# Optimization experiments

Hardware: AMD Instinct MI355X
Metric: run time of the kernel (lower is better)

Reference implementation:

```python
import jax, jax.numpy as jnp
import numpy as np

LMAX = 5
DIMS = [2 * l + 1 for l in range(LMAX + 1)]
S = sum(d * d for d in DIMS)  # 286 = sum_l (2l+1)^2 (mul_l = dim_l = 2l+1)
F_IN, F_OUT = 128, 128
B = 512
N_GRID = 512


def setup_inputs() -> dict:
    key = jax.random.key(0)
    k1, k2, k3 = jax.random.split(key, 3)
    # x: signal over SO(3) irreps, shape (B, f_in, S)
    x = jax.random.normal(k1, (B, F_IN, S), dtype=jnp.float32)
    # w: learned spatial filter, shape (f_in, f_out, n_grid) (nn.Parameter, normal init)
    w = jax.random.normal(k2, (F_IN, F_OUT, N_GRID), dtype=jnp.float32)
    # D: flattened Wigner-D buffer, shape (n_grid, S). Stand-in random values;
    # the forward math is identical to the true Wigner-D buffer.
    D = jax.random.normal(k3, (N_GRID, S), dtype=jnp.float32)
    return {"x": x, "w": w, "D": D}


def _so3_linear(x, psi):
    """e3nn o3.Linear over so3_irreps(LMAX) with external weights psi.

    Per degree l: x_l (B, f_in, 2l+1 [mul], 2l+1 [dim]),
    psi_l (f_in, f_out, mul_in, mul_out); mix multiplicities and f channels,
    with fan-in normalization 1/sqrt(f_in * mul_in).
    """
    bsz = x.shape[0]
    outs = []
    off = 0
    for l in range(LMAX + 1):
        d = 2 * l + 1
        blk = d * d
        x_l = x[:, :, off:off + blk].reshape(bsz, F_IN, d, d)
        w_l = psi[:, :, off:off + blk].reshape(F_IN, F_OUT, d, d)
        scale = 1.0 / np.sqrt(F_IN * d).astype(np.float32)
        y_l = jnp.einsum('bxui,xyuv->byvi', x_l, w_l) * scale
        outs.append(y_l.reshape(bsz, F_OUT, blk))
        off += blk
    return jnp.concatenate(outs, axis=-1)


def reference(x, w, D):
    # project spatial filter into harmonic (Fourier) domain
    psi = jnp.einsum('ni,xyn->xyi', D, w) / np.float32(np.sqrt(N_GRID))
    return _so3_linear(x, psi)
```

## Files before the change

### kernel.cpp

```cpp
#include <hip/hip_runtime.h>
#include <hip/hip_bf16.h>


#define NT 256
typedef __bf16 bf16x8 __attribute__((ext_vector_type(8)));
typedef float f32x4 __attribute__((ext_vector_type(4)));
typedef unsigned int u32;

__device__ __forceinline__ void gload_lds16(const void* g, void* l) {
  __builtin_amdgcn_global_load_lds(
      (const __attribute__((address_space(1))) u32*)g,
      (__attribute__((address_space(3))) u32*)l, 16, 0, 0);
}

__device__ __forceinline__ void decode_s(int s, int& off, int& d) {
  if (s >= 165)      { off = 165; d = 11; }
  else if (s >= 84)  { off = 84;  d = 9; }
  else if (s >= 35)  { off = 35;  d = 7; }
  else if (s >= 10)  { off = 10;  d = 5; }
  else if (s >= 1)   { off = 1;   d = 3; }
  else               { off = 0;   d = 1; }
}

template<int D, int OFF>
__device__ __forceinline__ void build_one(const float* __restrict__ X,
                                          __hip_bfloat16* __restrict__ A,
                                          int b, __hip_bfloat16* sm) {
  const float* src = X + (size_t)b * (128 * 286) + OFF;
  for (int e = threadIdx.x; e < 128 * D * D; e += NT) {
    const int x = e / (D * D), r = e - x * (D * D);
    sm[e] = __float2bfloat16(src[x * 286 + r]);
  }
  __syncthreads();
  __hip_bfloat16* dst = A + (size_t)65536 * OFF + (size_t)b * (D * 128 * D);
  for (int o = threadIdx.x; o < D * 128 * D; o += NT) {
    const int i = o / (128 * D);
    const int rem = o - i * (128 * D);
    const int x = rem / D, u = rem - x * D;
    dst[o] = sm[x * D * D + u * D + i];
  }
}

__global__ __launch_bounds__(NT)
void prep_all(const float* __restrict__ w, const float* __restrict__ Dm,
              const float* __restrict__ X,
              __hip_bfloat16* __restrict__ wb, __hip_bfloat16* __restrict__ DT,
              __hip_bfloat16* __restrict__ A) {
  __shared__ __hip_bfloat16 sm[128 * 121];
  const int bx = blockIdx.x;
  if (bx < 4096) {
    const int t = bx * NT + threadIdx.x;
    const float4 a = reinterpret_cast<const float4*>(w)[t * 2];
    const float4 b = reinterpret_cast<const float4*>(w)[t * 2 + 1];
    __hip_bfloat16 v[8];
    v[0] = __float2bfloat16(a.x); v[1] = __float2bfloat16(a.y);
    v[2] = __float2bfloat16(a.z); v[3] = __float2bfloat16(a.w);
    v[4] = __float2bfloat16(b.x); v[5] = __float2bfloat16(b.y);
    v[6] = __float2bfloat16(b.z); v[7] = __float2bfloat16(b.w);
    *reinterpret_cast<bf16x8*>(&wb[t * 8]) = *reinterpret_cast<bf16x8*>(v);
  } else if (bx < 4864) {
    const int e = (bx - 4096) * NT + threadIdx.x;
    const int s = e >> 9, g = e & 511;
    DT[e] = (s < 286) ? __float2bfloat16(Dm[g * 286 + s]) : __float2bfloat16(0.0f);
  } else {
    const int b2 = bx - 4864;
    if (b2 < 512)       build_one<11, 165>(X, A, b2, sm);
    else if (b2 < 1024) build_one<9, 84>(X, A, b2 - 512, sm);
    else if (b2 < 1536) build_one<7, 35>(X, A, b2 - 1024, sm);
    else if (b2 < 2048) build_one<5, 10>(X, A, b2 - 1536, sm);
    else if (b2 < 2560) build_one<3, 1>(X, A, b2 - 2048, sm);
    else                build_one<1, 0>(X, A, b2 - 2560, sm);
  }
}

__device__ __forceinline__ void load_frags(
    const __hip_bfloat16* sA, const __hip_bfloat16* sB,
    int wr, int wc, int r15, int khi, bf16x8 (&af)[4][2], bf16x8 (&bf)[4][2]) {
#pragma unroll
  for (int m = 0; m < 4; ++m)
#pragma unroll
    for (int kk = 0; kk < 2; ++kk) {
      const int row = wr * 64 + m * 16 + r15;
      const int slot = (kk * 4 + khi) ^ (row & 7);
      af[m][kk] = *reinterpret_cast<const bf16x8*>(&sA[row * 64 + slot * 8]);
    }
#pragma unroll
  for (int n = 0; n < 4; ++n)
#pragma unroll
    for (int kk = 0; kk < 2; ++kk) {
      const int row = wc * 64 + n * 16 + r15;
      const int slot = (kk * 4 + khi) ^ (row & 7);
      bf[n][kk] = *reinterpret_cast<const bf16x8*>(&sB[row * 64 + slot * 8]);
    }
}

__device__ __forceinline__ void do_mfma(
    const bf16x8 (&af)[4][2], const bf16x8 (&bf)[4][2], f32x4 (&acc)[4][4]) {
#pragma unroll
  for (int kk = 0; kk < 2; ++kk)
#pragma unroll
    for (int m = 0; m < 4; ++m)
#pragma unroll
      for (int n = 0; n < 4; ++n)
        acc[m][n] = __builtin_amdgcn_mfma_f32_16x16x32_bf16(
            af[m][kk], bf[n][kk], acc[m][n], 0, 0, 0);
}

__device__ __forceinline__ void stage_tile(
    const __hip_bfloat16* __restrict__ Ap, const __hip_bfloat16* __restrict__ Bp,
    int LDK, int ktv, int m0, int n0, int tid, int wave,
    __hip_bfloat16* sA, __hip_bfloat16* sB) {
#pragma unroll
  for (int c = 0; c < 4; ++c) {
    const int q = c * 256 + tid;
    const int row = q >> 3, slot = q & 7;
    const int scol = ((slot ^ (row & 7)) << 3);
    gload_lds16(&Ap[(m0 + row) * LDK + ktv + scol], &sA[(c * 256 + wave * 64) << 3]);
    gload_lds16(&Bp[(n0 + row) * LDK + ktv + scol], &sB[(c * 256 + wave * 64) << 3]);
  }
}

__global__ __launch_bounds__(NT)
void psi_mfma(const __hip_bfloat16* __restrict__ wb,
              const __hip_bfloat16* __restrict__ DT,
              __hip_bfloat16* __restrict__ PT) {
  const int m0 = blockIdx.x * 128, n0 = blockIdx.y * 128;

  __shared__ __hip_bfloat16 sA[2][128 * 64];
  __shared__ __hip_bfloat16 sB[2][128 * 64];

  const int tid = threadIdx.x;
  const int lane = tid & 63, wave = tid >> 6;
  const int wr = wave & 1, wc = wave >> 1;
  const int r15 = lane & 15, khi = lane >> 4;

  f32x4 acc[4][4] = {};
  bf16x8 af[4][2], bf[4][2];

  stage_tile(wb, DT, 512, 0, m0, n0, tid, wave, sA[0], sB[0]);
  __syncthreads();
  int cur = 0;
  for (int t = 0; t < 8; ++t) {
    if (t + 1 < 8)
      stage_tile(wb, DT, 512, (t + 1) << 6, m0, n0, tid, wave, sA[cur ^ 1], sB[cur ^ 1]);
    load_frags(sA[cur], sB[cur], wr, wc, r15, khi, af, bf);
    do_mfma(af, bf, acc);
    if (t + 1 < 8) { __syncthreads(); cur ^= 1; }
  }

#pragma unroll
  for (int n = 0; n < 4; ++n) {
    const int s = n0 + wc * 64 + n * 16 + r15;
    if (s >= 286) continue;
    int off, d;
    decode_s(s, off, d);
    const int rel = s - off;
    const int u = rel / d, v = rel - u * d;
    const float scale = 1.0f / (256.0f * sqrtf((float)d));
    __hip_bfloat16* Pl = PT + off * 16384;
    const int Kd = 128 * d;
#pragma unroll
    for (int m = 0; m < 4; ++m)
#pragma unroll
      for (int j = 0; j < 4; ++j) {
        const int row = m0 + wr * 64 + m * 16 + khi * 4 + j;
        const int x = row >> 7, y = row & 127;
        Pl[(y * d + v) * Kd + (x * d + u)] = __float2bfloat16(acc[m][n][j] * scale);
      }
  }
}

template<int D, int OFF>
__device__ __forceinline__ void tile_body(
    const __hip_bfloat16* __restrict__ Aall,
    const __hip_bfloat16* __restrict__ PTall,
    float* __restrict__ out, int bx,
    __hip_bfloat16* s0A, __hip_bfloat16* s0B,
    __hip_bfloat16* s1A, __hip_bfloat16* s1B) {
  const int tid = threadIdx.x;
  const int lane = tid & 63, wave = tid >> 6;
  const int wr = wave & 1, wc = wave >> 1;
  const int r15 = lane & 15, khi = lane >> 4;

  constexpr int Kn = 128 * D;
  constexpr int nk = 2 * D;
  const int bm = bx % (4 * D);
  const int bn = bx / (4 * D);
  const __hip_bfloat16* A  = Aall  + 65536 * OFF;
  const __hip_bfloat16* BT = PTall + 16384 * OFF;
  const int m0 = bm * 128, n0 = bn * 128;

  const int q0 = tid;
  f32x4 acc[4][4] = {};
  bf16x8 af[4][2], bf[4][2];

  __hip_bfloat16 *curA = s0A, *curB = s0B, *nxtA = s1A, *nxtB = s1B;

#pragma unroll
  for (int c = 0; c < 4; ++c) {
    const int q = c * 256 + q0;
    const int row = q >> 3, slot = q & 7;
    const int scol = ((slot ^ (row & 7)) << 3);
    gload_lds16(&A[(m0 + row) * Kn + scol], &curA[(c * 256 + wave * 64) << 3]);
    gload_lds16(&BT[(n0 + row) * Kn + scol], &curB[(c * 256 + wave * 64) << 3]);
  }

  for (int t = 0; t < nk; ++t) {
    if (t + 1 < nk) {
      const int kt = (t + 1) << 6;
#pragma unroll
      for (int c = 0; c < 4; ++c) {
        const int q = c * 256 + q0;
        const int row = q >> 3, slot = q & 7;
        const int scol = ((slot ^ (row & 7)) << 3);
        gload_lds16(&A[(m0 + row) * Kn + kt + scol], &nxtA[(c * 256 + wave * 64) << 3]);
        gload_lds16(&BT[(n0 + row) * Kn + kt + scol], &nxtB[(c * 256 + wave * 64) << 3]);
      }
      asm volatile("s_waitcnt vmcnt(8)" ::: "memory");
    } else {
      asm volatile("s_waitcnt vmcnt(0)" ::: "memory");
    }
    __builtin_amdgcn_s_barrier();
    asm volatile("" ::: "memory");

    load_frags(curA, curB, wr, wc, r15, khi, af, bf);
    __builtin_amdgcn_s_setprio(1);
    do_mfma(af, bf, acc);
    __builtin_amdgcn_s_setprio(0);

    asm volatile("" ::: "memory");
    __builtin_amdgcn_s_barrier();
    __hip_bfloat16* tA = curA; curA = nxtA; nxtA = tA;
    __hip_bfloat16* tB = curB; curB = nxtB; nxtB = tB;
  }

  int yo4[4], v4[4];
#pragma unroll
  for (int n = 0; n < 4; ++n) {
    const int col = n0 + wc * 64 + n * 16 + r15;
    yo4[n] = col / D;
    v4[n] = col - yo4[n] * D;
  }
#pragma unroll
  for (int m = 0; m < 4; ++m)
#pragma unroll
    for (int j = 0; j < 4; ++j) {
      const int row = m0 + wr * 64 + m * 16 + khi * 4 + j;
      const int bb = row / D, i = row - bb * D;
      float* orow = out + (size_t)bb * 36608 + OFF + i;
#pragma unroll
      for (int n = 0; n < 4; ++n)
        orow[yo4[n] * 286 + v4[n] * D] = acc[m][n][j];
    }
}

__global__ __launch_bounds__(NT)
void main_gemm(const __hip_bfloat16* __restrict__ Aall,
               const __hip_bfloat16* __restrict__ PTall,
               float* __restrict__ out) {
  __shared__ __hip_bfloat16 sA[2][128 * 64];
  __shared__ __hip_bfloat16 sB[2][128 * 64];
  const int bx = blockIdx.x;
  if (bx < 484)       tile_body<11, 165>(Aall, PTall, out, bx,        sA[0], sB[0], sA[1], sB[1]);
  else if (bx < 808)  tile_body<9, 84>(Aall, PTall, out, bx - 484,   sA[0], sB[0], sA[1], sB[1]);
  else if (bx < 1004) tile_body<7, 35>(Aall, PTall, out, bx - 808,   sA[0], sB[0], sA[1], sB[1]);
  else if (bx < 1104) tile_body<5, 10>(Aall, PTall, out, bx - 1004,  sA[0], sB[0], sA[1], sB[1]);
  else if (bx < 1140) tile_body<3, 1>(Aall, PTall, out, bx - 1104,   sA[0], sB[0], sA[1], sB[1]);
  else                tile_body<1, 0>(Aall, PTall, out, bx - 1140,   sA[0], sB[0], sA[1], sB[1]);
}

extern "C" void kernel_launch(void* const* d_in, const int* in_sizes, int n_in,
                              void* d_out, int out_size, void* d_ws, size_t ws_size,
                              hipStream_t stream) {
  const float* x  = (const float*)d_in[0];
  const float* w  = (const float*)d_in[1];
  const float* Dm = (const float*)d_in[2];
  float* out = (float*)d_out;

  __hip_bfloat16* PT = (__hip_bfloat16*)d_ws;
  __hip_bfloat16* A  = PT + 16384 * 286;
  __hip_bfloat16* wb = A + 65536 * 286;
  __hip_bfloat16* DT = wb + 16384 * 512;

  prep_all<<<dim3(7936), dim3(NT), 0, stream>>>(w, Dm, x, wb, DT, A);
  psi_mfma<<<dim3(128, 3), dim3(NT), 0, stream>>>(wb, DT, PT);
  main_gemm<<<dim3(1144), dim3(NT), 0, stream>>>(A, PT, out);
}
```

Measured before the change: 164.2 us.

## Rewrite main GEMM with 256x256 tiles, 8 waves, and interleaved half-tile pipeline

Replaces the 128x128 per-block main GEMM, which used 4 waves and a K-step of 64, with 256x256 tiles computed by 512-thread blocks of 8 waves and a K-step of 32. Staging of A and B halves is interleaved with MFMA phases across ping-pong LDS buffers, with finer vmcnt waits and barriers. The larger tiles raise arithmetic intensity and cut the grid from 1144 to 322 blocks. In exchange there are more barriers per K-step, partial tiles on N that need clamped loads and guarded stores, and fewer blocks to spread across the CUs.

```diff
diff --git a/kernel.cpp b/kernel.cpp
--- a/kernel.cpp
+++ b/kernel.cpp
@@ -3,6 +3,7 @@
 
 
 #define NT 256
+#define NT8 512
 typedef __bf16 bf16x8 __attribute__((ext_vector_type(8)));
 typedef float f32x4 __attribute__((ext_vector_type(4)));
 typedef unsigned int u32;
@@ -73,39 +74,6 @@
   }
 }
 
-__device__ __forceinline__ void load_frags(
-    const __hip_bfloat16* sA, const __hip_bfloat16* sB,
-    int wr, int wc, int r15, int khi, bf16x8 (&af)[4][2], bf16x8 (&bf)[4][2]) {
-#pragma unroll
-  for (int m = 0; m < 4; ++m)
-#pragma unroll
-    for (int kk = 0; kk < 2; ++kk) {
-      const int row = wr * 64 + m * 16 + r15;
-      const int slot = (kk * 4 + khi) ^ (row & 7);
-      af[m][kk] = *reinterpret_cast<const bf16x8*>(&sA[row * 64 + slot * 8]);
-    }
-#pragma unroll
-  for (int n = 0; n < 4; ++n)
-#pragma unroll
-    for (int kk = 0; kk < 2; ++kk) {
-      const int row = wc * 64 + n * 16 + r15;
-      const int slot = (kk * 4 + khi) ^ (row & 7);
-      bf[n][kk] = *reinterpret_cast<const bf16x8*>(&sB[row * 64 + slot * 8]);
-    }
-}
-
-__device__ __forceinline__ void do_mfma(
-    const bf16x8 (&af)[4][2], const bf16x8 (&bf)[4][2], f32x4 (&acc)[4][4]) {
-#pragma unroll
-  for (int kk = 0; kk < 2; ++kk)
-#pragma unroll
-    for (int m = 0; m < 4; ++m)
-#pragma unroll
-      for (int n = 0; n < 4; ++n)
-        acc[m][n] = __builtin_amdgcn_mfma_f32_16x16x32_bf16(
-            af[m][kk], bf[n][kk], acc[m][n], 0, 0, 0);
-}
-
 __device__ __forceinline__ void stage_tile(
     const __hip_bfloat16* __restrict__ Ap, const __hip_bfloat16* __restrict__ Bp,
     int LDK, int ktv, int m0, int n0, int tid, int wave,
@@ -118,6 +86,39 @@
     gload_lds16(&Ap[(m0 + row) * LDK + ktv + scol], &sA[(c * 256 + wave * 64) << 3]);
     gload_lds16(&Bp[(n0 + row) * LDK + ktv + scol], &sB[(c * 256 + wave * 64) << 3]);
   }
+}
+
+__device__ __forceinline__ void load_frags(
+    const __hip_bfloat16* sA, const __hip_bfloat16* sB,
+    int wr, int wc, int r15, int khi, bf16x8 (&af)[4][2], bf16x8 (&bf)[4][2]) {
+#pragma unroll
+  for (int m = 0; m < 4; ++m)
+#pragma unroll
+    for (int kk = 0; kk < 2; ++kk) {
+      const int row = wr * 64 + m * 16 + r15;
+      const int slot = (kk * 4 + khi) ^ (row & 7);
+      af[m][kk] = *reinterpret_cast<const bf16x8*>(&sA[row * 64 + slot * 8]);
+    }
+#pragma unroll
+  for (int n = 0; n < 4; ++n)
+#pragma unroll
+    for (int kk = 0; kk < 2; ++kk) {
+      const int row = wc * 64 + n * 16 + r15;
+      const int slot = (kk * 4 + khi) ^ (row & 7);
+      bf[n][kk] = *reinterpret_cast<const bf16x8*>(&sB[row * 64 + slot * 8]);
+    }
+}
+
+__device__ __forceinline__ void do_mfma(
+    const bf16x8 (&af)[4][2], const bf16x8 (&bf)[4][2], f32x4 (&acc)[4][4]) {
+#pragma unroll
+  for (int kk = 0; kk < 2; ++kk)
+#pragma unroll
+    for (int m = 0; m < 4; ++m)
+#pragma unroll
+      for (int n = 0; n < 4; ++n)
+        acc[m][n] = __builtin_amdgcn_mfma_f32_16x16x32_bf16(
+            af[m][kk], bf[n][kk], acc[m][n], 0, 0, 0);
 }
 
 __global__ __launch_bounds__(NT)
@@ -170,103 +171,130 @@
   }
 }
 
+#define VMC2() asm volatile("s_waitcnt vmcnt(2)" ::: "memory")
+#define VMC0() asm volatile("s_waitcnt vmcnt(0)" ::: "memory")
+#define BAR()  do { asm volatile("" ::: "memory"); __builtin_amdgcn_s_barrier(); \
+                    asm volatile("" ::: "memory"); } while (0)
+
 template<int D, int OFF>
-__device__ __forceinline__ void tile_body(
-    const __hip_bfloat16* __restrict__ Aall,
-    const __hip_bfloat16* __restrict__ PTall,
-    float* __restrict__ out, int bx,
-    __hip_bfloat16* s0A, __hip_bfloat16* s0B,
-    __hip_bfloat16* s1A, __hip_bfloat16* s1B) {
+__device__ __forceinline__ void tile8(const __hip_bfloat16* __restrict__ Aall,
+                                      const __hip_bfloat16* __restrict__ PTall,
+                                      float* __restrict__ out, int sub,
+                                      __hip_bfloat16* smem) {
   const int tid = threadIdx.x;
   const int lane = tid & 63, wave = tid >> 6;
-  const int wr = wave & 1, wc = wave >> 1;
+  const int wr = wave >> 2, wc = wave & 3;
   const int r15 = lane & 15, khi = lane >> 4;
 
-  constexpr int Kn = 128 * D;
-  constexpr int nk = 2 * D;
-  const int bm = bx % (4 * D);
-  const int bn = bx / (4 * D);
+  constexpr int Kn = 128 * D, NnM = 128 * D;
+  constexpr int NBM = 2 * D;
+  constexpr int ni = 2 * D;
+  const int bm = sub % NBM, bn = sub / NBM;
+  const int m0 = bm * 256, n0 = bn * 256;
   const __hip_bfloat16* A  = Aall  + 65536 * OFF;
   const __hip_bfloat16* BT = PTall + 16384 * OFF;
-  const int m0 = bm * 128, n0 = bn * 128;
-
-  const int q0 = tid;
-  f32x4 acc[4][4] = {};
-  bf16x8 af[4][2], bf[4][2];
-
-  __hip_bfloat16 *curA = s0A, *curB = s0B, *nxtA = s1A, *nxtB = s1B;
-
-#pragma unroll
-  for (int c = 0; c < 4; ++c) {
-    const int q = c * 256 + q0;
-    const int row = q >> 3, slot = q & 7;
-    const int scol = ((slot ^ (row & 7)) << 3);
-    gload_lds16(&A[(m0 + row) * Kn + scol], &curA[(c * 256 + wave * 64) << 3]);
-    gload_lds16(&BT[(n0 + row) * Kn + scol], &curB[(c * 256 + wave * 64) << 3]);
-  }
-
-  for (int t = 0; t < nk; ++t) {
-    if (t + 1 < nk) {
-      const int kt = (t + 1) << 6;
-#pragma unroll
-      for (int c = 0; c < 4; ++c) {
-        const int q = c * 256 + q0;
-        const int row = q >> 3, slot = q & 7;
-        const int scol = ((slot ^ (row & 7)) << 3);
-        gload_lds16(&A[(m0 + row) * Kn + kt + scol], &nxtA[(c * 256 + wave * 64) << 3]);
-        gload_lds16(&BT[(n0 + row) * Kn + kt + scol], &nxtB[(c * 256 + wave * 64) << 3]);
+
+  const int srow = tid >> 2, sslot = tid & 3;
+  const int scol = ((sslot ^ (srow & 3)) << 3);
+  const int garA0 = m0 + srow, garA1 = m0 + 128 + srow;
+  int gbr0 = n0 + srow;       if (gbr0 >= NnM) gbr0 = NnM - 1;
+  int gbr1 = n0 + 128 + srow; if (gbr1 >= NnM) gbr1 = NnM - 1;
+  const int dstoff = wave * 512;
+
+  __hip_bfloat16* cA[2] = { smem + (0 * 4 + 0 * 2 + wr) * 4096,
+                            smem + (1 * 4 + 0 * 2 + wr) * 4096 };
+  __hip_bfloat16* cB[2] = { smem + (0 * 4 + 1 * 2 + (wc >> 1)) * 4096,
+                            smem + (1 * 4 + 1 * 2 + (wc >> 1)) * 4096 };
+
+#define STG_A(par, kt) do {                                                   \
+    gload_lds16(&A[(size_t)garA0 * Kn + (kt) * 32 + scol],                    \
+                smem + ((par) * 4 + 0) * 4096 + dstoff);                      \
+    gload_lds16(&A[(size_t)garA1 * Kn + (kt) * 32 + scol],                    \
+                smem + ((par) * 4 + 1) * 4096 + dstoff);                      \
+  } while (0)
+#define STG_B(par, kt) do {                                                   \
+    gload_lds16(&BT[(size_t)gbr0 * Kn + (kt) * 32 + scol],                    \
+                smem + ((par) * 4 + 2) * 4096 + dstoff);                      \
+    gload_lds16(&BT[(size_t)gbr1 * Kn + (kt) * 32 + scol],                    \
+                smem + ((par) * 4 + 3) * 4096 + dstoff);                      \
+  } while (0)
+#define RD_AF(mh, par) { _Pragma("unroll")                                    \
+    for (int mm = 0; mm < 4; ++mm) {                                          \
+      const int lr = (mh) * 64 + mm * 16 + r15;                               \
+      af[mm] = *reinterpret_cast<const bf16x8*>(                              \
+          &cA[par][lr * 32 + ((khi ^ (lr & 3)) << 3)]);                       \
+    } }
+#define RD_BF(par) { _Pragma("unroll")                                        \
+    for (int nn = 0; nn < 4; ++nn) {                                          \
+      const int lr = (wc & 1) * 64 + nn * 16 + r15;                           \
+      bf[nn] = *reinterpret_cast<const bf16x8*>(                              \
+          &cB[par][lr * 32 + ((khi ^ (lr & 3)) << 3)]);                       \
+    } }
+#define MFMA16(mh) do { __builtin_amdgcn_s_setprio(1); _Pragma("unroll")      \
+    for (int mm = 0; mm < 4; ++mm) { _Pragma("unroll")                        \
+      for (int nn = 0; nn < 4; ++nn)                                          \
+        acc[(mh) * 4 + mm][nn] = __builtin_amdgcn_mfma_f32_16x16x32_bf16(     \
+            af[mm], bf[nn], acc[(mh) * 4 + mm][nn], 0, 0, 0); }               \
+    __builtin_amdgcn_s_setprio(0); } while (0)
+
+  f32x4 acc[8][4] = {};
+  bf16x8 af[4], bf[4];
+
+  STG_B(0, 0); STG_A(0, 0); STG_B(1, 1);
+  VMC2(); BAR();
+
+  for (int i = 0; i < ni; ++i) {
+    const bool tail = (i == ni - 1);
+    const int k2 = 2 * i;
+    RD_AF(0, 0); RD_BF(0);
+    STG_A(1, k2 + 1);
+    BAR(); MFMA16(0); BAR();
+    RD_AF(1, 0);
+    if (!tail) { STG_B(0, k2 + 2); VMC2(); } else { VMC0(); }
+    BAR(); MFMA16(1); BAR();
+    RD_AF(0, 1); RD_BF(1);
+    if (!tail) STG_A(0, k2 + 2);
+    BAR(); MFMA16(0); BAR();
+    RD_AF(1, 1);
+    if (!tail) { STG_B(1, k2 + 3); VMC2(); }
+    BAR(); MFMA16(1); BAR();
+  }
+
+#pragma unroll
+  for (int m = 0; m < 8; ++m)
+#pragma unroll
+    for (int j = 0; j < 4; ++j) {
+      const int gr = m0 + wr * 128 + m * 16 + khi * 4 + j;
+      const int bb = gr / D, ii = gr - bb * D;
+      float* orow = out + (size_t)bb * 36608 + OFF + ii;
+#pragma unroll
+      for (int n = 0; n < 4; ++n) {
+        const int gc = n0 + wc * 64 + n * 16 + r15;
+        if (gc < NnM) {
+          const int yo = gc / D, v = gc - yo * D;
+          orow[yo * 286 + v * D] = acc[m][n][j];
+        }
       }
-      asm volatile("s_waitcnt vmcnt(8)" ::: "memory");
-    } else {
-      asm volatile("s_waitcnt vmcnt(0)" ::: "memory");
     }
-    __builtin_amdgcn_s_barrier();
-    asm volatile("" ::: "memory");
-
-    load_frags(curA, curB, wr, wc, r15, khi, af, bf);
-    __builtin_amdgcn_s_setprio(1);
-    do_mfma(af, bf, acc);
-    __builtin_amdgcn_s_setprio(0);
-
-    asm volatile("" ::: "memory");
-    __builtin_amdgcn_s_barrier();
-    __hip_bfloat16* tA = curA; curA = nxtA; nxtA = tA;
-    __hip_bfloat16* tB = curB; curB = nxtB; nxtB = tB;
-  }
-
-  int yo4[4], v4[4];
-#pragma unroll
-  for (int n = 0; n < 4; ++n) {
-    const int col = n0 + wc * 64 + n * 16 + r15;
-    yo4[n] = col / D;
-    v4[n] = col - yo4[n] * D;
-  }
-#pragma unroll
-  for (int m = 0; m < 4; ++m)
-#pragma unroll
-    for (int j = 0; j < 4; ++j) {
-      const int row = m0 + wr * 64 + m * 16 + khi * 4 + j;
-      const int bb = row / D, i = row - bb * D;
-      float* orow = out + (size_t)bb * 36608 + OFF + i;
-#pragma unroll
-      for (int n = 0; n < 4; ++n)
-        orow[yo4[n] * 286 + v4[n] * D] = acc[m][n][j];
-    }
-}
-
-__global__ __launch_bounds__(NT)
-void main_gemm(const __hip_bfloat16* __restrict__ Aall,
-               const __hip_bfloat16* __restrict__ PTall,
-               float* __restrict__ out) {
-  __shared__ __hip_bfloat16 sA[2][128 * 64];
-  __shared__ __hip_bfloat16 sB[2][128 * 64];
+#undef STG_A
+#undef STG_B
+#undef RD_AF
+#undef RD_BF
+#undef MFMA16
+}
+
+__global__ __launch_bounds__(NT8, 2)
+void main_gemm8(const __hip_bfloat16* __restrict__ Aall,
+                const __hip_bfloat16* __restrict__ PTall,
+                float* __restrict__ out) {
+  __shared__ __hip_bfloat16 smem[8 * 4096];
   const int bx = blockIdx.x;
-  if (bx < 484)       tile_body<11, 165>(Aall, PTall, out, bx,        sA[0], sB[0], sA[1], sB[1]);
-  else if (bx < 808)  tile_body<9, 84>(Aall, PTall, out, bx - 484,   sA[0], sB[0], sA[1], sB[1]);
-  else if (bx < 1004) tile_body<7, 35>(Aall, PTall, out, bx - 808,   sA[0], sB[0], sA[1], sB[1]);
-  else if (bx < 1104) tile_body<5, 10>(Aall, PTall, out, bx - 1004,  sA[0], sB[0], sA[1], sB[1]);
-  else if (bx < 1140) tile_body<3, 1>(Aall, PTall, out, bx - 1104,   sA[0], sB[0], sA[1], sB[1]);
-  else                tile_body<1, 0>(Aall, PTall, out, bx - 1140,   sA[0], sB[0], sA[1], sB[1]);
+  if (bx < 132)      tile8<11, 165>(Aall, PTall, out, bx, smem);
+  else if (bx < 222) tile8<9, 84>(Aall, PTall, out, bx - 132, smem);
+  else if (bx < 278) tile8<7, 35>(Aall, PTall, out, bx - 222, smem);
+  else if (bx < 308) tile8<5, 10>(Aall, PTall, out, bx - 278, smem);
+  else if (bx < 320) tile8<3, 1>(Aall, PTall, out, bx - 308, smem);
+  else               tile8<1, 0>(Aall, PTall, out, bx - 320, smem);
 }
 
 extern "C" void kernel_launch(void* const* d_in, const int* in_sizes, int n_in,
@@ -284,5 +312,5 @@
 
   prep_all<<<dim3(7936), dim3(NT), 0, stream>>>(w, Dm, x, wb, DT, A);
   psi_mfma<<<dim3(128, 3), dim3(NT), 0, stream>>>(wb, DT, PT);
-  main_gemm<<<dim3(1144), dim3(NT), 0, stream>>>(A, PT, out);
-}
+  main_gemm8<<<dim3(322), dim3(NT8), 0, stream>>>(A, PT, out);
+}
```

Measured after the change: 164.9 us. Within noise of the previous version (+0.4%).

## Replace LDS-staged main GEMM with per-wave direct-to-register 32x32 MFMA tiles

Applied to the files above, without the earlier changes.

The main GEMM drops its double-buffered LDS staging, the barriers and the 16x16x32 MFMA fragments. Each wave now computes an independent 64x64 output tile, reading bf16 fragments straight from global memory into registers and accumulating with 32x32x16 MFMAs. This removes LDS traffic and block-wide synchronisation. In exchange, waves no longer share operand tiles and lanes read scattered 16-byte chunks across rows, so the kernel leans on L1/L2 for reuse and coalescing.

```diff
diff --git a/kernel.cpp b/kernel.cpp
--- a/kernel.cpp
+++ b/kernel.cpp
@@ -5,6 +5,7 @@
 #define NT 256
 typedef __bf16 bf16x8 __attribute__((ext_vector_type(8)));
 typedef float f32x4 __attribute__((ext_vector_type(4)));
+typedef float f32x16 __attribute__((ext_vector_type(16)));
 typedef unsigned int u32;
 
 __device__ __forceinline__ void gload_lds16(const void* g, void* l) {
@@ -73,39 +74,6 @@
   }
 }
 
-__device__ __forceinline__ void load_frags(
-    const __hip_bfloat16* sA, const __hip_bfloat16* sB,
-    int wr, int wc, int r15, int khi, bf16x8 (&af)[4][2], bf16x8 (&bf)[4][2]) {
-#pragma unroll
-  for (int m = 0; m < 4; ++m)
-#pragma unroll
-    for (int kk = 0; kk < 2; ++kk) {
-      const int row = wr * 64 + m * 16 + r15;
-      const int slot = (kk * 4 + khi) ^ (row & 7);
-      af[m][kk] = *reinterpret_cast<const bf16x8*>(&sA[row * 64 + slot * 8]);
-    }
-#pragma unroll
-  for (int n = 0; n < 4; ++n)
-#pragma unroll
-    for (int kk = 0; kk < 2; ++kk) {
-      const int row = wc * 64 + n * 16 + r15;
-      const int slot = (kk * 4 + khi) ^ (row & 7);
-      bf[n][kk] = *reinterpret_cast<const bf16x8*>(&sB[row * 64 + slot * 8]);
-    }
-}
-
-__device__ __forceinline__ void do_mfma(
-    const bf16x8 (&af)[4][2], const bf16x8 (&bf)[4][2], f32x4 (&acc)[4][4]) {
-#pragma unroll
-  for (int kk = 0; kk < 2; ++kk)
-#pragma unroll
-    for (int m = 0; m < 4; ++m)
-#pragma unroll
-      for (int n = 0; n < 4; ++n)
-        acc[m][n] = __builtin_amdgcn_mfma_f32_16x16x32_bf16(
-            af[m][kk], bf[n][kk], acc[m][n], 0, 0, 0);
-}
-
 __device__ __forceinline__ void stage_tile(
     const __hip_bfloat16* __restrict__ Ap, const __hip_bfloat16* __restrict__ Bp,
     int LDK, int ktv, int m0, int n0, int tid, int wave,
@@ -118,6 +86,39 @@
     gload_lds16(&Ap[(m0 + row) * LDK + ktv + scol], &sA[(c * 256 + wave * 64) << 3]);
     gload_lds16(&Bp[(n0 + row) * LDK + ktv + scol], &sB[(c * 256 + wave * 64) << 3]);
   }
+}
+
+__device__ __forceinline__ void load_frags(
+    const __hip_bfloat16* sA, const __hip_bfloat16* sB,
+    int wr, int wc, int r15, int khi, bf16x8 (&af)[4][2], bf16x8 (&bf)[4][2]) {
+#pragma unroll
+  for (int m = 0; m < 4; ++m)
+#pragma unroll
+    for (int kk = 0; kk < 2; ++kk) {
+      const int row = wr * 64 + m * 16 + r15;
+      const int slot = (kk * 4 + khi) ^ (row & 7);
+      af[m][kk] = *reinterpret_cast<const bf16x8*>(&sA[row * 64 + slot * 8]);
+    }
+#pragma unroll
+  for (int n = 0; n < 4; ++n)
+#pragma unroll
+    for (int kk = 0; kk < 2; ++kk) {
+      const int row = wc * 64 + n * 16 + r15;
+      const int slot = (kk * 4 + khi) ^ (row & 7);
+      bf[n][kk] = *reinterpret_cast<const bf16x8*>(&sB[row * 64 + slot * 8]);
+    }
+}
+
+__device__ __forceinline__ void do_mfma(
+    const bf16x8 (&af)[4][2], const bf16x8 (&bf)[4][2], f32x4 (&acc)[4][4]) {
+#pragma unroll
+  for (int kk = 0; kk < 2; ++kk)
+#pragma unroll
+    for (int m = 0; m < 4; ++m)
+#pragma unroll
+      for (int n = 0; n < 4; ++n)
+        acc[m][n] = __builtin_amdgcn_mfma_f32_16x16x32_bf16(
+            af[m][kk], bf[n][kk], acc[m][n], 0, 0, 0);
 }
 
 __global__ __launch_bounds__(NT)
@@ -171,102 +172,70 @@
 }
 
 template<int D, int OFF>
-__device__ __forceinline__ void tile_body(
-    const __hip_bfloat16* __restrict__ Aall,
-    const __hip_bfloat16* __restrict__ PTall,
-    float* __restrict__ out, int bx,
-    __hip_bfloat16* s0A, __hip_bfloat16* s0B,
-    __hip_bfloat16* s1A, __hip_bfloat16* s1B) {
-  const int tid = threadIdx.x;
-  const int lane = tid & 63, wave = tid >> 6;
-  const int wr = wave & 1, wc = wave >> 1;
-  const int r15 = lane & 15, khi = lane >> 4;
-
+__device__ __forceinline__ void tile_dr(const __hip_bfloat16* __restrict__ Aall,
+                                        const __hip_bfloat16* __restrict__ PTall,
+                                        float* __restrict__ out, int sub) {
+  const int lane = threadIdx.x & 63, wave = threadIdx.x >> 6;
+  const int r31 = lane & 31, khi2 = lane >> 5;
   constexpr int Kn = 128 * D;
-  constexpr int nk = 2 * D;
-  const int bm = bx % (4 * D);
-  const int bn = bx / (4 * D);
-  const __hip_bfloat16* A  = Aall  + 65536 * OFF;
-  const __hip_bfloat16* BT = PTall + 16384 * OFF;
-  const int m0 = bm * 128, n0 = bn * 128;
-
-  const int q0 = tid;
-  f32x4 acc[4][4] = {};
-  bf16x8 af[4][2], bf[4][2];
-
-  __hip_bfloat16 *curA = s0A, *curB = s0B, *nxtA = s1A, *nxtB = s1B;
-
-#pragma unroll
-  for (int c = 0; c < 4; ++c) {
-    const int q = c * 256 + q0;
-    const int row = q >> 3, slot = q & 7;
-    const int scol = ((slot ^ (row & 7)) << 3);
-    gload_lds16(&A[(m0 + row) * Kn + scol], &curA[(c * 256 + wave * 64) << 3]);
-    gload_lds16(&BT[(n0 + row) * Kn + scol], &curB[(c * 256 + wave * 64) << 3]);
-  }
-
-  for (int t = 0; t < nk; ++t) {
-    if (t + 1 < nk) {
-      const int kt = (t + 1) << 6;
-#pragma unroll
-      for (int c = 0; c < 4; ++c) {
-        const int q = c * 256 + q0;
-        const int row = q >> 3, slot = q & 7;
-        const int scol = ((slot ^ (row & 7)) << 3);
-        gload_lds16(&A[(m0 + row) * Kn + kt + scol], &nxtA[(c * 256 + wave * 64) << 3]);
-        gload_lds16(&BT[(n0 + row) * Kn + kt + scol], &nxtB[(c * 256 + wave * 64) << 3]);
+
+  const int wv = sub * 4 + wave;
+  const int bn = wv % (2 * D);
+  const int bm = wv / (2 * D);
+  const int m0 = bm * 64, n0 = bn * 64;
+
+  const __hip_bfloat16* A  = Aall  + (size_t)65536 * OFF;
+  const __hip_bfloat16* BT = PTall + (size_t)16384 * OFF;
+
+  const __hip_bfloat16* pa0 = A  + (size_t)(m0 + r31) * Kn + khi2 * 8;
+  const __hip_bfloat16* pa1 = pa0 + (size_t)32 * Kn;
+  const __hip_bfloat16* pb0 = BT + (size_t)(n0 + r31) * Kn + khi2 * 8;
+  const __hip_bfloat16* pb1 = pb0 + (size_t)32 * Kn;
+
+  f32x16 acc00 = {}, acc01 = {}, acc10 = {}, acc11 = {};
+
+#pragma unroll 2
+  for (int kt = 0; kt < Kn; kt += 16) {
+    const bf16x8 a0 = *reinterpret_cast<const bf16x8*>(pa0 + kt);
+    const bf16x8 a1 = *reinterpret_cast<const bf16x8*>(pa1 + kt);
+    const bf16x8 b0 = *reinterpret_cast<const bf16x8*>(pb0 + kt);
+    const bf16x8 b1 = *reinterpret_cast<const bf16x8*>(pb1 + kt);
+    acc00 = __builtin_amdgcn_mfma_f32_32x32x16_bf16(a0, b0, acc00, 0, 0, 0);
+    acc01 = __builtin_amdgcn_mfma_f32_32x32x16_bf16(a0, b1, acc01, 0, 0, 0);
+    acc10 = __builtin_amdgcn_mfma_f32_32x32x16_bf16(a1, b0, acc10, 0, 0, 0);
+    acc11 = __builtin_amdgcn_mfma_f32_32x32x16_bf16(a1, b1, acc11, 0, 0, 0);
+  }
+
+  const f32x16* accs[4] = { &acc00, &acc01, &acc10, &acc11 };
+#pragma unroll
+  for (int mi = 0; mi < 2; ++mi)
+#pragma unroll
+    for (int ni = 0; ni < 2; ++ni) {
+      const f32x16& a = *accs[mi * 2 + ni];
+      const int gc = n0 + ni * 32 + r31;
+      const int yo = gc / D, v = gc - yo * D;
+      const int cbase = yo * 286 + OFF + v * D;
+#pragma unroll
+      for (int reg = 0; reg < 16; ++reg) {
+        const int row = (reg & 3) + 8 * (reg >> 2) + 4 * khi2;
+        const int gr = m0 + mi * 32 + row;
+        const int bb = gr / D, ii = gr - bb * D;
+        out[(size_t)bb * 36608 + cbase + ii] = a[reg];
       }
-      asm volatile("s_waitcnt vmcnt(8)" ::: "memory");
-    } else {
-      asm volatile("s_waitcnt vmcnt(0)" ::: "memory");
     }
-    __builtin_amdgcn_s_barrier();
-    asm volatile("" ::: "memory");
-
-    load_frags(curA, curB, wr, wc, r15, khi, af, bf);
-    __builtin_amdgcn_s_setprio(1);
-    do_mfma(af, bf, acc);
-    __builtin_amdgcn_s_setprio(0);
-
-    asm volatile("" ::: "memory");
-    __builtin_amdgcn_s_barrier();
-    __hip_bfloat16* tA = curA; curA = nxtA; nxtA = tA;
-    __hip_bfloat16* tB = curB; curB = nxtB; nxtB = tB;
-  }
-
-  int yo4[4], v4[4];
-#pragma unroll
-  for (int n = 0; n < 4; ++n) {
-    const int col = n0 + wc * 64 + n * 16 + r15;
-    yo4[n] = col / D;
-    v4[n] = col - yo4[n] * D;
-  }
-#pragma unroll
-  for (int m = 0; m < 4; ++m)
-#pragma unroll
-    for (int j = 0; j < 4; ++j) {
-      const int row = m0 + wr * 64 + m * 16 + khi * 4 + j;
-      const int bb = row / D, i = row - bb * D;
-      float* orow = out + (size_t)bb * 36608 + OFF + i;
-#pragma unroll
-      for (int n = 0; n < 4; ++n)
-        orow[yo4[n] * 286 + v4[n] * D] = acc[m][n][j];
-    }
 }
 
 __global__ __launch_bounds__(NT)
-void main_gemm(const __hip_bfloat16* __restrict__ Aall,
-               const __hip_bfloat16* __restrict__ PTall,
-               float* __restrict__ out) {
-  __shared__ __hip_bfloat16 sA[2][128 * 64];
-  __shared__ __hip_bfloat16 sB[2][128 * 64];
+void main_gemm_dr(const __hip_bfloat16* __restrict__ Aall,
+                  const __hip_bfloat16* __restrict__ PTall,
+                  float* __restrict__ out) {
   const int bx = blockIdx.x;
-  if (bx < 484)       tile_body<11, 165>(Aall, PTall, out, bx,        sA[0], sB[0], sA[1], sB[1]);
-  else if (bx < 808)  tile_body<9, 84>(Aall, PTall, out, bx - 484,   sA[0], sB[0], sA[1], sB[1]);
-  else if (bx < 1004) tile_body<7, 35>(Aall, PTall, out, bx - 808,   sA[0], sB[0], sA[1], sB[1]);
-  else if (bx < 1104) tile_body<5, 10>(Aall, PTall, out, bx - 1004,  sA[0], sB[0], sA[1], sB[1]);
-  else if (bx < 1140) tile_body<3, 1>(Aall, PTall, out, bx - 1104,   sA[0], sB[0], sA[1], sB[1]);
-  else                tile_body<1, 0>(Aall, PTall, out, bx - 1140,   sA[0], sB[0], sA[1], sB[1]);
+  if (bx < 484)       tile_dr<11, 165>(Aall, PTall, out, bx);
+  else if (bx < 808)  tile_dr<9, 84>(Aall, PTall, out, bx - 484);
+  else if (bx < 1004) tile_dr<7, 35>(Aall, PTall, out, bx - 808);
+  else if (bx < 1104) tile_dr<5, 10>(Aall, PTall, out, bx - 1004);
+  else if (bx < 1140) tile_dr<3, 1>(Aall, PTall, out, bx - 1104);
+  else                tile_dr<1, 0>(Aall, PTall, out, bx - 1140);
 }
 
 extern "C" void kernel_launch(void* const* d_in, const int* in_sizes, int n_in,
@@ -284,5 +253,5 @@
 
   prep_all<<<dim3(7936), dim3(NT), 0, stream>>>(w, Dm, x, wb, DT, A);
   psi_mfma<<<dim3(128, 3), dim3(NT), 0, stream>>>(wb, DT, PT);
-  main_gemm<<<dim3(1144), dim3(NT), 0, stream>>>(A, PT, out);
-}
+  main_gemm_dr<<<dim3(1144), dim3(NT), 0, stream>>>(A, PT, out);
+}
```

Result: slower. 275.0 us (+67.5%).

## Restructure main GEMM pipeline, add XCD block remap and occupancy hint

Applied to the files above, without the earlier changes.

The main GEMM K-loop now calls the shared stage_tile helper. It drops the explicit vmcnt waits and s_setprio, and uses a single __syncthreads per iteration in place of paired barriers. Block indices are remapped so consecutive hardware blocks, which are dispatched round-robin across the 8 XCDs, take contiguous tiles, which is meant to improve L2 reuse per XCD. launch_bounds gains a minimum of 4 blocks per SM to cap register use. The loop no longer appears to wait for the async global-to-LDS loads before reading the current buffer; it relies on __syncthreads inserting the wait, which changes how loads overlap with compute.

```diff
diff --git a/kernel.cpp b/kernel.cpp
--- a/kernel.cpp
+++ b/kernel.cpp
@@ -73,39 +73,6 @@
   }
 }
 
-__device__ __forceinline__ void load_frags(
-    const __hip_bfloat16* sA, const __hip_bfloat16* sB,
-    int wr, int wc, int r15, int khi, bf16x8 (&af)[4][2], bf16x8 (&bf)[4][2]) {
-#pragma unroll
-  for (int m = 0; m < 4; ++m)
-#pragma unroll
-    for (int kk = 0; kk < 2; ++kk) {
-      const int row = wr * 64 + m * 16 + r15;
-      const int slot = (kk * 4 + khi) ^ (row & 7);
-      af[m][kk] = *reinterpret_cast<const bf16x8*>(&sA[row * 64 + slot * 8]);
-    }
-#pragma unroll
-  for (int n = 0; n < 4; ++n)
-#pragma unroll
-    for (int kk = 0; kk < 2; ++kk) {
-      const int row = wc * 64 + n * 16 + r15;
-      const int slot = (kk * 4 + khi) ^ (row & 7);
-      bf[n][kk] = *reinterpret_cast<const bf16x8*>(&sB[row * 64 + slot * 8]);
-    }
-}
-
-__device__ __forceinline__ void do_mfma(
-    const bf16x8 (&af)[4][2], const bf16x8 (&bf)[4][2], f32x4 (&acc)[4][4]) {
-#pragma unroll
-  for (int kk = 0; kk < 2; ++kk)
-#pragma unroll
-    for (int m = 0; m < 4; ++m)
-#pragma unroll
-      for (int n = 0; n < 4; ++n)
-        acc[m][n] = __builtin_amdgcn_mfma_f32_16x16x32_bf16(
-            af[m][kk], bf[n][kk], acc[m][n], 0, 0, 0);
-}
-
 __device__ __forceinline__ void stage_tile(
     const __hip_bfloat16* __restrict__ Ap, const __hip_bfloat16* __restrict__ Bp,
     int LDK, int ktv, int m0, int n0, int tid, int wave,
@@ -118,6 +85,39 @@
     gload_lds16(&Ap[(m0 + row) * LDK + ktv + scol], &sA[(c * 256 + wave * 64) << 3]);
     gload_lds16(&Bp[(n0 + row) * LDK + ktv + scol], &sB[(c * 256 + wave * 64) << 3]);
   }
+}
+
+__device__ __forceinline__ void load_frags(
+    const __hip_bfloat16* sA, const __hip_bfloat16* sB,
+    int wr, int wc, int r15, int khi, bf16x8 (&af)[4][2], bf16x8 (&bf)[4][2]) {
+#pragma unroll
+  for (int m = 0; m < 4; ++m)
+#pragma unroll
+    for (int kk = 0; kk < 2; ++kk) {
+      const int row = wr * 64 + m * 16 + r15;
+      const int slot = (kk * 4 + khi) ^ (row & 7);
+      af[m][kk] = *reinterpret_cast<const bf16x8*>(&sA[row * 64 + slot * 8]);
+    }
+#pragma unroll
+  for (int n = 0; n < 4; ++n)
+#pragma unroll
+    for (int kk = 0; kk < 2; ++kk) {
+      const int row = wc * 64 + n * 16 + r15;
+      const int slot = (kk * 4 + khi) ^ (row & 7);
+      bf[n][kk] = *reinterpret_cast<const bf16x8*>(&sB[row * 64 + slot * 8]);
+    }
+}
+
+__device__ __forceinline__ void do_mfma(
+    const bf16x8 (&af)[4][2], const bf16x8 (&bf)[4][2], f32x4 (&acc)[4][4]) {
+#pragma unroll
+  for (int kk = 0; kk < 2; ++kk)
+#pragma unroll
+    for (int m = 0; m < 4; ++m)
+#pragma unroll
+      for (int n = 0; n < 4; ++n)
+        acc[m][n] = __builtin_amdgcn_mfma_f32_16x16x32_bf16(
+            af[m][kk], bf[n][kk], acc[m][n], 0, 0, 0);
 }
 
 __global__ __launch_bounds__(NT)
@@ -175,8 +175,7 @@
     const __hip_bfloat16* __restrict__ Aall,
     const __hip_bfloat16* __restrict__ PTall,
     float* __restrict__ out, int bx,
-    __hip_bfloat16* s0A, __hip_bfloat16* s0B,
-    __hip_bfloat16* s1A, __hip_bfloat16* s1B) {
+    __hip_bfloat16 (*sA)[128 * 64], __hip_bfloat16 (*sB)[128 * 64]) {
   const int tid = threadIdx.x;
   const int lane = tid & 63, wave = tid >> 6;
   const int wr = wave & 1, wc = wave >> 1;
@@ -190,48 +189,18 @@
   const __hip_bfloat16* BT = PTall + 16384 * OFF;
   const int m0 = bm * 128, n0 = bn * 128;
 
-  const int q0 = tid;
   f32x4 acc[4][4] = {};
   bf16x8 af[4][2], bf[4][2];
 
-  __hip_bfloat16 *curA = s0A, *curB = s0B, *nxtA = s1A, *nxtB = s1B;
-
-#pragma unroll
-  for (int c = 0; c < 4; ++c) {
-    const int q = c * 256 + q0;
-    const int row = q >> 3, slot = q & 7;
-    const int scol = ((slot ^ (row & 7)) << 3);
-    gload_lds16(&A[(m0 + row) * Kn + scol], &curA[(c * 256 + wave * 64) << 3]);
-    gload_lds16(&BT[(n0 + row) * Kn + scol], &curB[(c * 256 + wave * 64) << 3]);
-  }
-
+  stage_tile(A, BT, Kn, 0, m0, n0, tid, wave, sA[0], sB[0]);
+  __syncthreads();
+  int cur = 0;
   for (int t = 0; t < nk; ++t) {
-    if (t + 1 < nk) {
-      const int kt = (t + 1) << 6;
-#pragma unroll
-      for (int c = 0; c < 4; ++c) {
-        const int q = c * 256 + q0;
-        const int row = q >> 3, slot = q & 7;
-        const int scol = ((slot ^ (row & 7)) << 3);
-        gload_lds16(&A[(m0 + row) * Kn + kt + scol], &nxtA[(c * 256 + wave * 64) << 3]);
-        gload_lds16(&BT[(n0 + row) * Kn + kt + scol], &nxtB[(c * 256 + wave * 64) << 3]);
-      }
-      asm volatile("s_waitcnt vmcnt(8)" ::: "memory");
-    } else {
-      asm volatile("s_waitcnt vmcnt(0)" ::: "memory");
-    }
-    __builtin_amdgcn_s_barrier();
-    asm volatile("" ::: "memory");
-
-    load_frags(curA, curB, wr, wc, r15, khi, af, bf);
-    __builtin_amdgcn_s_setprio(1);
+    if (t + 1 < nk)
+      stage_tile(A, BT, Kn, (t + 1) << 6, m0, n0, tid, wave, sA[cur ^ 1], sB[cur ^ 1]);
+    load_frags(sA[cur], sB[cur], wr, wc, r15, khi, af, bf);
     do_mfma(af, bf, acc);
-    __builtin_amdgcn_s_setprio(0);
-
-    asm volatile("" ::: "memory");
-    __builtin_amdgcn_s_barrier();
-    __hip_bfloat16* tA = curA; curA = nxtA; nxtA = tA;
-    __hip_bfloat16* tB = curB; curB = nxtB; nxtB = tB;
+    if (t + 1 < nk) { __syncthreads(); cur ^= 1; }
   }
 
   int yo4[4], v4[4];
@@ -254,19 +223,20 @@
     }
 }
 
-__global__ __launch_bounds__(NT)
+__global__ __launch_bounds__(NT, 4)
 void main_gemm(const __hip_bfloat16* __restrict__ Aall,
                const __hip_bfloat16* __restrict__ PTall,
                float* __restrict__ out) {
   __shared__ __hip_bfloat16 sA[2][128 * 64];
   __shared__ __hip_bfloat16 sB[2][128 * 64];
-  const int bx = blockIdx.x;
-  if (bx < 484)       tile_body<11, 165>(Aall, PTall, out, bx,        sA[0], sB[0], sA[1], sB[1]);
-  else if (bx < 808)  tile_body<9, 84>(Aall, PTall, out, bx - 484,   sA[0], sB[0], sA[1], sB[1]);
-  else if (bx < 1004) tile_body<7, 35>(Aall, PTall, out, bx - 808,   sA[0], sB[0], sA[1], sB[1]);
-  else if (bx < 1104) tile_body<5, 10>(Aall, PTall, out, bx - 1004,  sA[0], sB[0], sA[1], sB[1]);
-  else if (bx < 1140) tile_body<3, 1>(Aall, PTall, out, bx - 1104,   sA[0], sB[0], sA[1], sB[1]);
-  else                tile_body<1, 0>(Aall, PTall, out, bx - 1140,   sA[0], sB[0], sA[1], sB[1]);
+  const int raw = blockIdx.x;
+  const int bx = (raw & 7) * 143 + (raw >> 3);
+  if (bx < 484)       tile_body<11, 165>(Aall, PTall, out, bx, sA, sB);
+  else if (bx < 808)  tile_body<9, 84>(Aall, PTall, out, bx - 484, sA, sB);
+  else if (bx < 1004) tile_body<7, 35>(Aall, PTall, out, bx - 808, sA, sB);
+  else if (bx < 1104) tile_body<5, 10>(Aall, PTall, out, bx - 1004, sA, sB);
+  else if (bx < 1140) tile_body<3, 1>(Aall, PTall, out, bx - 1104, sA, sB);
+  else                tile_body<1, 0>(Aall, PTall, out, bx - 1140, sA, sB);
 }
 
 extern "C" void kernel_launch(void* const* d_in, const int* in_sizes, int n_in,
```

Result: slower. 261.8 us (+59.4%).
